# Kernel tuning notes

Hardware: AMD Instinct MI355X
Metric: run time of the kernel (lower is better)

Reference implementation:

```python
import jax, jax.numpy as jnp
import numpy as np

B, N, D, H = 2048, 200, 128, 8

def setup_inputs() -> dict:
    key = jax.random.key(0)
    k1, k2, k3, k4, k5, k6 = jax.random.split(key, 6)
    return {
        "item_embedding": jax.random.normal(k1, (B, N, D), dtype=jnp.float32),
        "query_embedding": jax.random.normal(k2, (B, D), dtype=jnp.float32),
        "mask": jax.random.randint(k3, (B, N, 1), 0, 2).astype(bool),
        "Wq": jax.random.normal(k4, (D * H, D), dtype=jnp.float32) * 0.05,
        "bq": jax.random.normal(k5, (D * H,), dtype=jnp.float32) * 0.05,
        "Wr": jax.random.normal(k6, (1, H), dtype=jnp.float32) * 0.5,
    }

def reference(item_embedding, query_embedding, mask, Wq, bq, Wr):
    b = query_embedding.shape[0]
    # query projection + tanh, reshape to (B, D, H)
    pq = jnp.tanh(query_embedding @ Wq.T + bq).reshape(b, D, H)
    # batched dot: (B,N,D) @ (B,D,H) -> (B,N,H)
    dotted = jnp.einsum('bnd,bdh->bnh', item_embedding, pq)
    # head reduce: (B,N,H) @ (H,1) -> (B,N,1)
    reduced = dotted @ Wr.T
    scores = reduced - jnp.max(reduced, axis=1, keepdims=True)
    att = jnp.exp(scores) * mask
    denom = jnp.sum(att, axis=1, keepdims=True)
    weight = att / jnp.where(denom < 1e-7, denom + 1.0, denom)
    # weighted sum pooling -> (B, D)
    return jnp.sum(weight * item_embedding, axis=1)
```

## Files before the change

### kernel.cpp

```cpp
#include <hip/hip_runtime.h>

#define BB 2048
#define NN 200
#define DD 128
#define HH 8

typedef float f4v __attribute__((ext_vector_type(4)));

__global__ __launch_bounds__(256) void proj_kernel(
    const float* __restrict__ q,
    const float* __restrict__ Wq,
    const float* __restrict__ bq,
    const float* __restrict__ Wr,
    float* __restrict__ v)
{
    __shared__ float wq_s[32][257];
    const int t  = threadIdx.x;
    const int jc = blockIdx.x;
    const int b0 = blockIdx.y * 16;
    const int j  = jc * 256 + t;

    float acc[16];
#pragma unroll
    for (int i = 0; i < 16; ++i) acc[i] = 0.f;

    for (int kt = 0; kt < 4; ++kt) {
        __syncthreads();
#pragma unroll
        for (int i = 0; i < 8; ++i) {
            int idx = t + 256 * i;
            int jj  = idx >> 3;
            int kf  = idx & 7;
            const float4 w4 = *(const float4*)(Wq + (size_t)(jc*256 + jj)*128 + kt*32 + kf*4);
            wq_s[kf*4+0][jj] = w4.x;
            wq_s[kf*4+1][jj] = w4.y;
            wq_s[kf*4+2][jj] = w4.z;
            wq_s[kf*4+3][jj] = w4.w;
        }
        __syncthreads();

        float wreg[32];
#pragma unroll
        for (int k = 0; k < 32; ++k) wreg[k] = wq_s[k][t];

#pragma unroll
        for (int bb = 0; bb < 16; ++bb) {
            const float* qrow = q + (size_t)(b0 + bb)*128 + kt*32;
            float s = 0.f;
#pragma unroll
            for (int k = 0; k < 32; ++k) s = fmaf(qrow[k], wreg[k], s);
            acc[bb] += s;
        }
    }

    const float bqj = bq[j];
    const float wrh = Wr[j & 7];
    const int   d   = j >> 3;
#pragma unroll
    for (int bb = 0; bb < 16; ++bb) {
        float p = tanhf(acc[bb] + bqj) * wrh;
        p += __shfl_xor(p, 1);
        p += __shfl_xor(p, 2);
        p += __shfl_xor(p, 4);
        if ((t & 7) == 0) v[(size_t)(b0 + bb)*128 + d] = p;
    }
}

__global__ __launch_bounds__(512, 8) void attn_kernel(
    const float* __restrict__ item,
    const int*   __restrict__ mask,
    const float* __restrict__ v,
    float* __restrict__ out)
{
    __shared__ float  mask_s[NN];
    __shared__ float2 ml_s[16];
    __shared__ __align__(16) float stage[16][132];

    const int t    = threadIdx.x;
    const int b    = blockIdx.x;
    const int seg  = t & 31;
    const int half = t >> 5;

    const f4v vreg = *(const f4v*)(v + (size_t)b*128 + seg*4);
    const float* itemb = item + (size_t)b * (NN * 128);

    if (t < NN) mask_s[t] = mask[(size_t)b * NN + t] ? 1.f : 0.f;

    f4v pre[5];
#pragma unroll
    for (int i = 0; i < 5; ++i) {
        const int row = half + 16*i;
        pre[i] = (f4v)0.f;
        if (row < 64)
            pre[i] = *(const f4v*)(itemb + (size_t)row*128 + seg*4);
    }
    __syncthreads();

    float mh = -3e38f, lh = 0.f;
    f4v oh = (f4v)0.f;

    for (int c = 0; c < 3; ++c) {
        const int base = c * 64;
        const int rows = (c == 2) ? 72 : 64;

        float pp[5];
#pragma unroll
        for (int i = 0; i < 5; ++i) {
            const f4v f = pre[i];
            float s = f[0]*vreg[0] + f[1]*vreg[1] + f[2]*vreg[2] + f[3]*vreg[3];
#pragma unroll
            for (int off = 16; off >= 1; off >>= 1)
                s += __shfl_xor(s, off);
            pp[i] = s;
        }

        float mn = mh;
#pragma unroll
        for (int i = 0; i < 5; ++i)
            if (half + 16*i < rows) mn = fmaxf(mn, pp[i]);

        const float alpha = __expf(mh - mn);
        mh = mn;
        lh *= alpha;
        oh[0] *= alpha; oh[1] *= alpha; oh[2] *= alpha; oh[3] *= alpha;

#pragma unroll
        for (int i = 0; i < 5; ++i) {
            const int row = half + 16*i;
            if (row < rows) {
                const float w = mask_s[base + row] * __expf(pp[i] - mn);
                lh += w;
                oh[0] = fmaf(w, pre[i][0], oh[0]);
                oh[1] = fmaf(w, pre[i][1], oh[1]);
                oh[2] = fmaf(w, pre[i][2], oh[2]);
                oh[3] = fmaf(w, pre[i][3], oh[3]);
            }
        }

        if (c < 2) {
            const int nbase = (c + 1) * 64;
            const int nrows = (c == 1) ? 72 : 64;
#pragma unroll
            for (int i = 0; i < 5; ++i) {
                const int row = half + 16*i;
                pre[i] = (f4v)0.f;
                if (row < nrows)
                    pre[i] = *(const f4v*)(itemb + (size_t)(nbase + row)*128 + seg*4);
            }
        }
    }

    if (seg == 0) ml_s[half] = make_float2(mh, lh);
    *(f4v*)(&stage[half][seg*4]) = oh;
    __syncthreads();

    if (t < 128) {
        float mg = -3e38f;
#pragma unroll
        for (int h = 0; h < 16; ++h) mg = fmaxf(mg, ml_s[h].x);
        float lsum = 0.f, tot = 0.f;
#pragma unroll
        for (int h = 0; h < 16; ++h) {
            const float sc = __expf(ml_s[h].x - mg);
            lsum += ml_s[h].y * sc;
            tot  = fmaf(stage[h][t], sc, tot);
        }
        const float denom = (lsum < 1e-7f) ? (lsum + 1.f) : lsum;
        out[(size_t)b * 128 + t] = tot / denom;
    }
}

extern "C" void kernel_launch(void* const* d_in, const int* in_sizes, int n_in,
                              void* d_out, int out_size, void* d_ws, size_t ws_size,
                              hipStream_t stream) {
    const float* item = (const float*)d_in[0];
    const float* q    = (const float*)d_in[1];
    const int*   mask = (const int*)  d_in[2];
    const float* Wq   = (const float*)d_in[3];
    const float* bq   = (const float*)d_in[4];
    const float* Wr   = (const float*)d_in[5];
    float* out = (float*)d_out;
    float* v   = (float*)d_ws;

    proj_kernel<<<dim3(4, 128), 256, 0, stream>>>(q, Wq, bq, Wr, v);
    attn_kernel<<<dim3(BB), 512, 0, stream>>>(item, mask, v, out);
}
```

Measured before the change: 344.9 us.

## Issue all item loads upfront with nontemporal hints and relax occupancy bound

```diff
diff --git a/kernel.cpp b/kernel.cpp
--- a/kernel.cpp
+++ b/kernel.cpp
@@ -66,7 +66,7 @@
     }
 }
 
-__global__ __launch_bounds__(512, 8) void attn_kernel(
+__global__ __launch_bounds__(512, 3) void attn_kernel(
     const float* __restrict__ item,
     const int*   __restrict__ mask,
     const float* __restrict__ v,
@@ -86,69 +86,64 @@
 
     if (t < NN) mask_s[t] = mask[(size_t)b * NN + t] ? 1.f : 0.f;
 
-    f4v pre[5];
+    f4v pre0[5], pre1[5], pre2[5];
 #pragma unroll
     for (int i = 0; i < 5; ++i) {
         const int row = half + 16*i;
-        pre[i] = (f4v)0.f;
-        if (row < 64)
-            pre[i] = *(const f4v*)(itemb + (size_t)row*128 + seg*4);
+        pre0[i] = (f4v)0.f; pre1[i] = (f4v)0.f; pre2[i] = (f4v)0.f;
+        if (row < 64) {
+            pre0[i] = __builtin_nontemporal_load(
+                (const f4v*)(itemb + (size_t)row*128        + seg*4));
+            pre1[i] = __builtin_nontemporal_load(
+                (const f4v*)(itemb + (size_t)(64 + row)*128 + seg*4));
+        }
+        if (row < 72)
+            pre2[i] = __builtin_nontemporal_load(
+                (const f4v*)(itemb + (size_t)(128 + row)*128 + seg*4));
     }
     __syncthreads();
 
     float mh = -3e38f, lh = 0.f;
     f4v oh = (f4v)0.f;
 
-    for (int c = 0; c < 3; ++c) {
-        const int base = c * 64;
-        const int rows = (c == 2) ? 72 : 64;
+#define CHUNK_BODY(PRE, BASE, ROWS)                                          \
+    {                                                                        \
+        float pp[5];                                                         \
+        _Pragma("unroll")                                                    \
+        for (int i = 0; i < 5; ++i) {                                        \
+            const f4v f = PRE[i];                                            \
+            float s = f[0]*vreg[0] + f[1]*vreg[1] + f[2]*vreg[2] + f[3]*vreg[3]; \
+            _Pragma("unroll")                                                \
+            for (int off = 16; off >= 1; off >>= 1)                          \
+                s += __shfl_xor(s, off);                                     \
+            pp[i] = s;                                                       \
+        }                                                                    \
+        float mn = mh;                                                       \
+        _Pragma("unroll")                                                    \
+        for (int i = 0; i < 5; ++i)                                          \
+            if (half + 16*i < (ROWS)) mn = fmaxf(mn, pp[i]);                 \
+        const float alpha = __expf(mh - mn);                                 \
+        mh = mn;                                                             \
+        lh *= alpha;                                                         \
+        oh[0] *= alpha; oh[1] *= alpha; oh[2] *= alpha; oh[3] *= alpha;      \
+        _Pragma("unroll")                                                    \
+        for (int i = 0; i < 5; ++i) {                                        \
+            const int row = half + 16*i;                                     \
+            if (row < (ROWS)) {                                              \
+                const float w = mask_s[(BASE) + row] * __expf(pp[i] - mn);   \
+                lh += w;                                                     \
+                oh[0] = fmaf(w, PRE[i][0], oh[0]);                           \
+                oh[1] = fmaf(w, PRE[i][1], oh[1]);                           \
+                oh[2] = fmaf(w, PRE[i][2], oh[2]);                           \
+                oh[3] = fmaf(w, PRE[i][3], oh[3]);                           \
+            }                                                                \
+        }                                                                    \
+    }
 
-        float pp[5];
-#pragma unroll
-        for (int i = 0; i < 5; ++i) {
-            const f4v f = pre[i];
-            float s = f[0]*vreg[0] + f[1]*vreg[1] + f[2]*vreg[2] + f[3]*vreg[3];
-#pragma unroll
-            for (int off = 16; off >= 1; off >>= 1)
-                s += __shfl_xor(s, off);
-            pp[i] = s;
-        }
-
-        float mn = mh;
-#pragma unroll
-        for (int i = 0; i < 5; ++i)
-            if (half + 16*i < rows) mn = fmaxf(mn, pp[i]);
-
-        const float alpha = __expf(mh - mn);
-        mh = mn;
-        lh *= alpha;
-        oh[0] *= alpha; oh[1] *= alpha; oh[2] *= alpha; oh[3] *= alpha;
-
-#pragma unroll
-        for (int i = 0; i < 5; ++i) {
-            const int row = half + 16*i;
-            if (row < rows) {
-                const float w = mask_s[base + row] * __expf(pp[i] - mn);
-                lh += w;
-                oh[0] = fmaf(w, pre[i][0], oh[0]);
-                oh[1] = fmaf(w, pre[i][1], oh[1]);
-                oh[2] = fmaf(w, pre[i][2], oh[2]);
-                oh[3] = fmaf(w, pre[i][3], oh[3]);
-            }
-        }
-
-        if (c < 2) {
-            const int nbase = (c + 1) * 64;
-            const int nrows = (c == 1) ? 72 : 64;
-#pragma unroll
-            for (int i = 0; i < 5; ++i) {
-                const int row = half + 16*i;
-                pre[i] = (f4v)0.f;
-                if (row < nrows)
-                    pre[i] = *(const f4v*)(itemb + (size_t)(nbase + row)*128 + seg*4);
-            }
-        }
-    }
+    CHUNK_BODY(pre0,   0, 64)
+    CHUNK_BODY(pre1,  64, 64)
+    CHUNK_BODY(pre2, 128, 72)
+#undef CHUNK_BODY
 
     if (seg == 0) ml_s[half] = make_float2(mh, lh);
     *(f4v*)(&stage[half][seg*4]) = oh;
```

Result: faster. 329.4 us (-4.5%).
